# Performance work log

Measured on AMD Instinct MI355X. Metric: run time of the kernel, lower is better.

Reference implementation:

```python
import jax, jax.numpy as jnp
import numpy as np

B, S, H, D = 8, 1024, 8, 64      # batch, seq_len, num_heads, num_hidden
DM = H * D                        # input model dim = 512
DK = 64.0                         # d_k scale
EPS = 1e-3                        # keras GroupNormalization default epsilon


def setup_inputs() -> dict:
    key = jax.random.key(0)
    ks = jax.random.split(key, 12)
    sc = 1.0 / np.sqrt(DM)
    return {
        "query":  jax.random.normal(ks[0], (B, S, DM), jnp.float32),
        "key":    jax.random.normal(ks[1], (B, S, DM), jnp.float32),
        "values": jax.random.normal(ks[2], (B, S, DM), jnp.float32),
        "Wq": jax.random.normal(ks[3], (DM, 3 * H * D), jnp.float32) * sc,
        "bq": jnp.zeros((3 * H * D,), jnp.float32),
        "Wk": jax.random.normal(ks[4], (DM, 2 * H * D), jnp.float32) * sc,
        "bk": jnp.zeros((2 * H * D,), jnp.float32),
        "Wv": jax.random.normal(ks[5], (DM, H * D), jnp.float32) * sc,
        "bv": jnp.zeros((H * D,), jnp.float32),
        "gamma": jnp.ones((D,), jnp.float32),
        "beta": jnp.zeros((D,), jnp.float32),
        "lam": jax.random.uniform(ks[6], (1,), jnp.float32),          # trainable lambda
        "lambda_init": jax.random.uniform(ks[7], (1,), jnp.float32),  # frozen lambda_init
    }


def reference(query, key, values, Wq, bq, Wk, bk, Wv, bv, gamma, beta, lam, lambda_init):
    # projections -> (B, H, S, *)
    q = (query @ Wq + bq).reshape(B, S, H, 3 * D).transpose(0, 2, 1, 3)
    k = (key @ Wk + bk).reshape(B, S, H, 2 * D).transpose(0, 2, 1, 3)
    v = (values @ Wv + bv).reshape(B, S, H, D).transpose(0, 2, 1, 3)

    q1, q2, gate = jnp.split(q, 3, axis=-1)      # each (B,H,S,D)
    k1, k2 = k[..., :D], k[..., D:]

    inv = 1.0 / jnp.sqrt(jnp.float32(DK))
    s1 = jnp.einsum("bhqd,bhkd->bhqk", q1, k1) * inv
    s2 = jnp.einsum("bhqd,bhkd->bhqk", q2, k2) * inv

    # differential attention: dual softmax combined with learned lambda
    attn = jax.nn.softmax(s1, axis=-1) - lam[0] * jax.nn.softmax(s2, axis=-1)
    out = jnp.einsum("bhqk,bhkd->bhqd", attn, v)      # (B,H,S,D)
    out = out.transpose(0, 2, 1, 3)                    # (B,S,H,D)

    # keras GroupNormalization(groups=H, axis=-1) on channels D:
    # reshape channel dim into (groups, D//H), reduce over all non-batch,
    # non-group axes: (S, H, D//H)
    g = out.reshape(B, S, H, H, D // H)
    mean = jnp.mean(g, axis=(1, 2, 4), keepdims=True)
    var = jnp.var(g, axis=(1, 2, 4), keepdims=True)
    g = (g - mean) * jax.lax.rsqrt(var + EPS)
    out = g.reshape(B, S, H, D) * gamma + beta

    out = out * (1.0 - lambda_init[0])
    out = out * jax.nn.sigmoid(gate.transpose(0, 2, 1, 3))
    return out.reshape(B, S, H * D)
```

## Files before the change

### kernel.cpp

```cpp
#include <hip/hip_runtime.h>
#include <cstdint>
#include <cstddef>

#define B_ 8
#define S_ 1024
#define H_ 8
#define D_ 64
#define DM_ 512

typedef __bf16 bf16x8 __attribute__((ext_vector_type(8)));
typedef float floatx4 __attribute__((ext_vector_type(4)));
typedef float floatx16 __attribute__((ext_vector_type(16)));
typedef unsigned short ushort8 __attribute__((ext_vector_type(8)));
typedef unsigned short ushort4v __attribute__((ext_vector_type(4)));
typedef unsigned int uint32x2 __attribute__((ext_vector_type(2)));

union Frag { ushort8 us; bf16x8 bf; };

#define MFMA16(a, b, c) __builtin_amdgcn_mfma_f32_16x16x32_bf16((a), (b), (c), 0, 0, 0)
#define MFMA32(a, b, c) __builtin_amdgcn_mfma_f32_32x32x16_bf16((a), (b), (c), 0, 0, 0)

__device__ __forceinline__ unsigned short f2bf(float f) {
  unsigned int u = __float_as_uint(f);
  unsigned int r = (u + 0x7fffu + ((u >> 16) & 1u)) >> 16;
  return (unsigned short)r;
}

__device__ __forceinline__ uint32_t cvtpk_bf16(float lo, float hi) {
  uint32_t r;
  asm("v_cvt_pk_bf16_f32 %0, %1, %2" : "=v"(r) : "v"(lo), "v"(hi));
  return r;
}

__device__ __forceinline__ void gload16(const void* g, void* l) {
  __builtin_amdgcn_global_load_lds(
      (const __attribute__((address_space(1))) unsigned int*)g,
      (__attribute__((address_space(3))) unsigned int*)l, 16, 0, 0);
}

__global__ __launch_bounds__(256) void prep_kernel(
    const float* __restrict__ q, const float* __restrict__ k,
    const float* __restrict__ v, unsigned short* __restrict__ abf,
    const float* __restrict__ Wq, const float* __restrict__ Wk,
    const float* __restrict__ Wv, unsigned short* __restrict__ wt,
    float* __restrict__ partial)
{
  __shared__ unsigned short sT[64][72];
  const int tid = threadIdx.x;
  if (blockIdx.x < 2048) {
    const int t = blockIdx.x * 256 + tid;
    #pragma unroll
    for (int i = 0; i < 6; i++) {
      size_t i4 = ((size_t)i * 524288 + t) * 4;
      const size_t SEG = (size_t)4 << 20;
      const float* src = (i4 < SEG) ? (q + i4)
                       : (i4 < 2 * SEG) ? (k + (i4 - SEG))
                                        : (v + (i4 - 2 * SEG));
      floatx4 f = *(const floatx4*)src;
      ushort4v o;
      o[0] = f2bf(f[0]); o[1] = f2bf(f[1]); o[2] = f2bf(f[2]); o[3] = f2bf(f[3]);
      *(ushort4v*)(abf + i4) = o;
    }
    return;
  }
  if (blockIdx.x == 2432) {
    if (tid < 128) partial[tid] = 0.f;
    return;
  }
  const int bid = blockIdx.x - 2048;
  const int k0 = (bid & 7) * 64;
  const int n0 = (bid >> 3) * 64;
  const float* src; int ncols, nb;
  if (n0 < 1536)      { src = Wq; ncols = 1536; nb = n0; }
  else if (n0 < 2560) { src = Wk; ncols = 1024; nb = n0 - 1536; }
  else                { src = Wv; ncols = 512;  nb = n0 - 2560; }

  const int kr0 = tid >> 4, nc4 = (tid & 15) * 4;
  #pragma unroll
  for (int i = 0; i < 4; i++) {
    int kr = kr0 + i * 16;
    floatx4 f = *(const floatx4*)(src + (size_t)(k0 + kr) * ncols + nb + nc4);
    sT[nc4 + 0][kr] = f2bf(f[0]);
    sT[nc4 + 1][kr] = f2bf(f[1]);
    sT[nc4 + 2][kr] = f2bf(f[2]);
    sT[nc4 + 3][kr] = f2bf(f[3]);
  }
  __syncthreads();
  const int nr0 = tid >> 3, kc8 = (tid & 7) * 8;
  #pragma unroll
  for (int i = 0; i < 2; i++) {
    int nr = nr0 + i * 32;
    *(ushort8*)(wt + (size_t)(n0 + nr) * 512 + k0 + kc8) = *(const ushort8*)&sT[nr][kc8];
  }
}

__global__ __launch_bounds__(256) void gemm_kernel(
    const unsigned short* __restrict__ abf, const unsigned short* __restrict__ wt,
    const float* __restrict__ bq, const float* __restrict__ bk,
    const float* __restrict__ bv,
    unsigned short* __restrict__ q1, unsigned short* __restrict__ q2,
    float* __restrict__ gate, unsigned short* __restrict__ k1,
    unsigned short* __restrict__ k2, unsigned short* __restrict__ vT)
{
  const int tid  = threadIdx.x;
  const int wave = tid >> 6;
  const int lane = tid & 63;
  const int l16  = lane & 15;
  const int quad = lane >> 4;
  const int mt = blockIdx.x;
  const int nt = blockIdx.y;
  const int wm = wave & 1, wn = wave >> 1;

  const unsigned short* Asrc =
      abf + (nt < 12 ? 0 : nt < 20 ? ((size_t)4 << 20) : ((size_t)8 << 20));

  __shared__ unsigned short sMem[4 * 128 * 64];

  floatx4 acc[4][4];
  #pragma unroll
  for (int i = 0; i < 4; i++)
    #pragma unroll
    for (int j = 0; j < 4; j++)
      #pragma unroll
      for (int r = 0; r < 4; r++) acc[i][j][r] = 0.0f;

  const int lrow   = lane >> 3;
  const int gchunk = (lane & 7) ^ lrow;
  const int rkey   = l16 & 7;

  auto STAGE = [&](int kt, int buf) {
    unsigned short* sA = sMem + buf * 16384;
    unsigned short* sB = sA + 8192;
    #pragma unroll
    for (int j = 0; j < 4; j++) {
      int r8 = (wave * 4 + j) * 8;
      gload16(Asrc + (size_t)(mt * 128 + r8 + lrow) * 512 + kt * 64 + gchunk * 8,
              &sA[(wave * 4 + j) * 512]);
      gload16(wt + (size_t)(nt * 128 + r8 + lrow) * 512 + kt * 64 + gchunk * 8,
              &sB[(wave * 4 + j) * 512]);
    }
  };

  auto COMPUTE = [&](int buf) {
    unsigned short* sA = sMem + buf * 16384;
    unsigned short* sB = sA + 8192;
    #pragma unroll
    for (int c = 0; c < 2; c++) {
      Frag af[4], bf[4];
      #pragma unroll
      for (int mi = 0; mi < 4; mi++)
        af[mi].us = *(const ushort8*)&sA[(wm * 64 + mi * 16 + l16) * 64 +
                                         (((c * 4 + quad) ^ rkey) << 3)];
      #pragma unroll
      for (int ni = 0; ni < 4; ni++)
        bf[ni].us = *(const ushort8*)&sB[(wn * 64 + ni * 16 + l16) * 64 +
                                         (((c * 4 + quad) ^ rkey) << 3)];
      __builtin_amdgcn_s_setprio(1);
      #pragma unroll
      for (int mi = 0; mi < 4; mi++)
        #pragma unroll
        for (int ni = 0; ni < 4; ni++)
          acc[mi][ni] = MFMA16(af[mi].bf, bf[ni].bf, acc[mi][ni]);
      __builtin_amdgcn_s_setprio(0);
    }
  };

  STAGE(0, 0);
  asm volatile("s_waitcnt vmcnt(0)" ::: "memory");
  __builtin_amdgcn_s_barrier();
  for (int kt = 0; kt < 8; kt++) {
    if (kt < 7) STAGE(kt + 1, (kt + 1) & 1);
    COMPUTE(kt & 1);
    asm volatile("s_waitcnt vmcnt(0) lgkmcnt(0)" ::: "memory");
    __builtin_amdgcn_s_barrier();
  }

  const int gm0 = mt * 128 + wm * 64;
  const int bb  = gm0 >> 10;
  const int s0  = gm0 & 1023;
  const int nseg = nt * 2 + wn;
  unsigned short* sC = sMem + wave * 4096;

  int h, sel = 0; bool isV = false;
  const float* bias_arr; int nb0;
  unsigned short* dstb = nullptr;
  if (nseg < 24)      { h = nseg / 3; sel = nseg % 3; bias_arr = bq; nb0 = nseg * 64;
                        dstb = (sel == 0) ? q1 : (sel == 1) ? q2 : nullptr; }
  else if (nseg < 40) { int t = nseg - 24; h = t >> 1; sel = t & 1;
                        bias_arr = bk; nb0 = t * 64; dstb = sel ? k2 : k1; }
  else                { h = nseg - 40; isV = true; bias_arr = bv; nb0 = (nseg - 40) * 64; }

  if (dstb != nullptr || isV) {
    const float scl = (nseg < 24) ? 0.125f * 1.44269504088896f : 1.0f;
    #pragma unroll
    for (int ni = 0; ni < 4; ni++) {
      float bv_ = bias_arr[nb0 + ni * 16 + l16];
      #pragma unroll
      for (int mi = 0; mi < 4; mi++)
        #pragma unroll
        for (int r = 0; r < 4; r++) {
          float val = (acc[mi][ni][r] + bv_) * scl;
          int ml = mi * 16 + quad * 4 + r;
          int nl = ni * 16 + l16;
          if (!isV) {
            int ch = (nl >> 3) ^ (ml & 7);
            sC[ml * 64 + (ch << 3) + (nl & 7)] = f2bf(val);
          } else {
            int ch = (ml >> 3) ^ (nl & 7);
            sC[nl * 64 + (ch << 3) + (ml & 7)] = f2bf(val);
          }
        }
    }
    const int rr = lane >> 3, cc = lane & 7;
    if (!isV) {
      unsigned short* base = dstb + ((size_t)(bb * H_ + h) * S_ + s0) * D_;
      #pragma unroll
      for (int j = 0; j < 8; j++) {
        int row = j * 8 + rr;
        int logc = cc ^ (row & 7);
        ushort8 valv = *(const ushort8*)&sC[row * 64 + cc * 8];
        *(ushort8*)(base + (size_t)row * D_ + logc * 8) = valv;
      }
    } else {
      unsigned short* base = vT + ((size_t)(bb * H_ + h) * D_) * S_ + s0;
      #pragma unroll
      for (int j = 0; j < 8; j++) {
        int drow = j * 8 + rr;
        int logc = cc ^ (drow & 7);
        ushort8 valv = *(const ushort8*)&sC[drow * 64 + cc * 8];
        *(ushort8*)(base + (size_t)drow * S_ + logc * 8) = valv;
      }
    }
  } else {
    #pragma unroll
    for (int ni = 0; ni < 4; ni++) {
      float bv_ = bias_arr[nb0 + ni * 16 + l16];
      #pragma unroll
      for (int mi = 0; mi < 4; mi++)
        #pragma unroll
        for (int r = 0; r < 4; r++) {
          int s = s0 + mi * 16 + quad * 4 + r;
          int d = ni * 16 + l16;
          gate[((size_t)(bb * H_ + h) * S_ + s) * D_ + d] = acc[mi][ni][r] + bv_;
        }
    }
  }
}

__global__ __launch_bounds__(256, 4) void attn_kernel(
    const unsigned short* __restrict__ q1, const unsigned short* __restrict__ q2,
    const unsigned short* __restrict__ k1, const unsigned short* __restrict__ k2,
    const unsigned short* __restrict__ vT, const float* __restrict__ lamp,
    float* __restrict__ O, float* __restrict__ partial)
{
  const int tid   = threadIdx.x;
  const int wave  = tid >> 6;
  const int lane  = tid & 63;
  const int l32   = lane & 31;
  const int lhalf = lane >> 5;
  const int kh    = wave & 1;
  const int qh    = wave >> 1;
  const int bh = blockIdx.x & 63;
  const int qt = blockIdx.x >> 6;
  const int q0 = qt * 64;

  __shared__ unsigned short sMem[5 * 4096];
  unsigned short* sK1 = sMem;
  unsigned short* sK2 = sMem + 4096;
  unsigned short* sVt = sMem + 8192;
  unsigned short* sP1 = sMem + 12288;
  unsigned short* sP2 = sMem + 16384;

  const size_t qrowoff = ((size_t)bh * S_ + q0 + qh * 32 + l32) * D_ + lhalf * 8;
  Frag qb1[4], qb2[4];
  #pragma unroll
  for (int ks = 0; ks < 4; ks++) {
    qb1[ks].us = *(const ushort8*)(q1 + qrowoff + ks * 16);
    qb2[ks].us = *(const ushort8*)(q2 + qrowoff + ks * 16);
  }

  floatx16 o1, o2;
  #pragma unroll
  for (int r = 0; r < 16; r++) { o1[r] = 0.f; o2[r] = 0.f; }
  float l1 = 0.f, l2 = 0.f;

  const unsigned short* kb1 = k1 + (size_t)bh * S_ * D_;
  const unsigned short* kb2 = k2 + (size_t)bh * S_ * D_;
  const unsigned short* vb  = vT + (size_t)bh * D_ * S_;

  const int srow = lane >> 3;
  const int sgch = (lane & 7) ^ srow;
  const int akey = l32 & 7;
  const int mrow = kh * 32 + l32;
  const int qrow = (qh * 32 + l32) * 64;

  auto STAGE_K = [&](int kt) {
    #pragma unroll
    for (int i = 0; i < 2; i++) {
      int r0 = wave * 16 + i * 8;
      gload16(kb1 + (size_t)(kt * 64 + r0 + srow) * 64 + sgch * 8, &sK1[r0 * 64]);
      gload16(kb2 + (size_t)(kt * 64 + r0 + srow) * 64 + sgch * 8, &sK2[r0 * 64]);
    }
  };
  auto STAGE_V = [&](int kt) {
    #pragma unroll
    for (int i = 0; i < 2; i++) {
      int r0 = wave * 16 + i * 8;
      gload16(vb + (size_t)(r0 + srow) * S_ + kt * 64 + sgch * 8, &sVt[r0 * 64]);
    }
  };

  auto S_PHASE = [&]() {
    floatx16 s1, s2;
    #pragma unroll
    for (int r = 0; r < 16; r++) { s1[r] = 0.f; s2[r] = 0.f; }
    __builtin_amdgcn_s_setprio(1);
    #pragma unroll
    for (int ks = 0; ks < 4; ks++) {
      int phys = ((ks * 2 + lhalf) ^ akey) << 3;
      Frag kf1; kf1.us = *(const ushort8*)&sK1[mrow * 64 + phys];
      s1 = MFMA32(kf1.bf, qb1[ks].bf, s1);
      Frag kf2; kf2.us = *(const ushort8*)&sK2[mrow * 64 + phys];
      s2 = MFMA32(kf2.bf, qb2[ks].bf, s2);
    }
    __builtin_amdgcn_s_setprio(0);
    #pragma unroll
    for (int qd = 0; qd < 4; qd++) {
      const int addr = qrow + (((kh * 4 + qd) ^ akey) << 3) + 4 * lhalf;
      float e0 = __builtin_amdgcn_exp2f(s1[4 * qd + 0]);
      float e1 = __builtin_amdgcn_exp2f(s1[4 * qd + 1]);
      float e2 = __builtin_amdgcn_exp2f(s1[4 * qd + 2]);
      float e3 = __builtin_amdgcn_exp2f(s1[4 * qd + 3]);
      l1 += (e0 + e1) + (e2 + e3);
      uint32x2 w1; w1[0] = cvtpk_bf16(e0, e1); w1[1] = cvtpk_bf16(e2, e3);
      *(uint32x2*)&sP1[addr] = w1;
      float f0 = __builtin_amdgcn_exp2f(s2[4 * qd + 0]);
      float f1 = __builtin_amdgcn_exp2f(s2[4 * qd + 1]);
      float f2 = __builtin_amdgcn_exp2f(s2[4 * qd + 2]);
      float f3 = __builtin_amdgcn_exp2f(s2[4 * qd + 3]);
      l2 += (f0 + f1) + (f2 + f3);
      uint32x2 w2; w2[0] = cvtpk_bf16(f0, f1); w2[1] = cvtpk_bf16(f2, f3);
      *(uint32x2*)&sP2[addr] = w2;
    }
  };

  auto PV_PHASE = [&]() {
    __builtin_amdgcn_s_setprio(1);
    #pragma unroll
    for (int ks = 0; ks < 4; ks++) {
      int phys = ((ks * 2 + lhalf) ^ akey) << 3;
      Frag vf; vf.us = *(const ushort8*)&sVt[mrow * 64 + phys];
      Frag pf1; pf1.us = *(const ushort8*)&sP1[qrow + phys];
      o1 = MFMA32(vf.bf, pf1.bf, o1);
      Frag pf2; pf2.us = *(const ushort8*)&sP2[qrow + phys];
      o2 = MFMA32(vf.bf, pf2.bf, o2);
    }
    __builtin_amdgcn_s_setprio(0);
  };

  STAGE_K(0);
  STAGE_V(0);
  asm volatile("s_waitcnt vmcnt(2)" ::: "memory");
  __builtin_amdgcn_s_barrier();
  S_PHASE();
  asm volatile("s_waitcnt vmcnt(0) lgkmcnt(0)" ::: "memory");
  __builtin_amdgcn_s_barrier();

  for (int kt = 1; kt < 16; kt++) {
    STAGE_K(kt);
    PV_PHASE();
    asm volatile("s_waitcnt lgkmcnt(0)" ::: "memory");
    __builtin_amdgcn_s_barrier();
    STAGE_V(kt);
    asm volatile("s_waitcnt vmcnt(2)" ::: "memory");
    __builtin_amdgcn_s_barrier();
    S_PHASE();
    asm volatile("s_waitcnt vmcnt(0) lgkmcnt(0)" ::: "memory");
    __builtin_amdgcn_s_barrier();
  }
  PV_PHASE();
  asm volatile("s_waitcnt lgkmcnt(0)" ::: "memory");
  __builtin_amdgcn_s_barrier();

  l1 += __shfl_xor(l1, 32, 64);
  l2 += __shfl_xor(l2, 32, 64);
  float* sL = (float*)(sMem + 10240);
  float* sG = (float*)(sMem + 10752);
  if (lane < 32) {
    sL[(0 * 2 + kh) * 64 + qh * 32 + l32] = l1;
    sL[(1 * 2 + kh) * 64 + qh * 32 + l32] = l2;
  }
  __syncthreads();

  const int q = qh * 32 + l32;
  float i1 = 1.0f / (sL[q] + sL[64 + q]);
  float i2 = lamp[0] / (sL[128 + q] + sL[192 + q]);
  float* fO = (float*)sMem;
  #pragma unroll
  for (int r = 0; r < 16; r++) {
    int d = kh * 32 + (r & 3) + 8 * (r >> 2) + 4 * lhalf;
    fO[d * 65 + q] = o1[r] * i1 - o2[r] * i2;
  }
  if (tid < 16) sG[tid] = 0.f;
  __syncthreads();

  float ss = 0.f, ss2 = 0.f;
  float* Ob = O + ((size_t)bh * S_ + q0) * D_;
  #pragma unroll
  for (int i = 0; i < 4; i++) {
    int qrw = i * 16 + (tid >> 4);
    int d0 = (tid & 15) * 4;
    floatx4 v;
    #pragma unroll
    for (int j = 0; j < 4; j++) {
      v[j] = fO[(d0 + j) * 65 + qrw];
      ss += v[j]; ss2 += v[j] * v[j];
    }
    *(floatx4*)(Ob + (size_t)qrw * D_ + d0) = v;
  }
  ss  += __shfl_xor(ss, 16, 64);  ss  += __shfl_xor(ss, 32, 64);  ss  += __shfl_xor(ss, 1, 64);
  ss2 += __shfl_xor(ss2, 16, 64); ss2 += __shfl_xor(ss2, 32, 64); ss2 += __shfl_xor(ss2, 1, 64);
  if (lane < 16 && (lane & 1) == 0) {
    int j = lane >> 1;
    atomicAdd(&sG[j * 2],     ss);
    atomicAdd(&sG[j * 2 + 1], ss2);
  }
  __syncthreads();
  if (tid < 16) atomicAdd(&partial[(bh >> 3) * 16 + tid], sG[tid]);
}

__global__ __launch_bounds__(256) void final_kernel(
    const float* __restrict__ O, const float* __restrict__ gate,
    const float* __restrict__ partial, const float* __restrict__ gamma,
    const float* __restrict__ beta, const float* __restrict__ li,
    float* __restrict__ out)
{
  const int t = blockIdx.x * 256 + threadIdx.x;
  const float li0 = 1.0f - li[0];
  #pragma unroll
  for (int it = 0; it < 2; it++) {
    int e4 = (it * 524288 + t) * 4;
    int d0 = e4 & 63;
    int hh = (e4 >> 6) & 7;
    int s  = (e4 >> 9) & 1023;
    int b  = e4 >> 19;
    size_t oidx = (size_t)(b * 8 + hh) * 65536 + (size_t)s * 64 + d0;
    int g = b * 8 + (d0 >> 3);
    float S1 = partial[g * 2];
    float S2 = partial[g * 2 + 1];
    float mean = S1 * (1.0f / 65536.f);
    float inv  = rsqrtf(S2 * (1.0f / 65536.f) - mean * mean + 0.001f);
    floatx4 o  = *(const floatx4*)(O + oidx);
    floatx4 gt = *(const floatx4*)(gate + oidx);
    floatx4 gm = *(const floatx4*)(gamma + d0);
    floatx4 bt = *(const floatx4*)(beta + d0);
    floatx4 r;
    #pragma unroll
    for (int j = 0; j < 4; j++) {
      float x = (o[j] - mean) * inv;
      x = x * gm[j] + bt[j];
      x *= li0;
      x *= 1.0f / (1.0f + __expf(-gt[j]));
      r[j] = x;
    }
    *(floatx4*)(out + e4) = r;
  }
}

extern "C" void kernel_launch(void* const* d_in, const int* in_sizes, int n_in,
                              void* d_out, int out_size, void* d_ws, size_t ws_size,
                              hipStream_t stream)
{
  const float* query  = (const float*)d_in[0];
  const float* key    = (const float*)d_in[1];
  const float* values = (const float*)d_in[2];
  const float* Wq = (const float*)d_in[3];
  const float* bq = (const float*)d_in[4];
  const float* Wk = (const float*)d_in[5];
  const float* bk = (const float*)d_in[6];
  const float* Wv = (const float*)d_in[7];
  const float* bv = (const float*)d_in[8];
  const float* gamma = (const float*)d_in[9];
  const float* beta  = (const float*)d_in[10];
  const float* lam   = (const float*)d_in[11];
  const float* lami  = (const float*)d_in[12];
  float* out = (float*)d_out;

  char* ws = (char*)d_ws;
  const size_t MB = (size_t)1 << 20;
  unsigned short* abf = (unsigned short*)(ws);
  float*          O   = (float*)(ws);
  unsigned short* wt  = (unsigned short*)(ws + 24 * MB);
  float* partial      = (float*)(ws + 27 * MB);
  unsigned short* q1  = (unsigned short*)(ws + 28 * MB);
  unsigned short* q2  = (unsigned short*)(ws + 36 * MB);
  unsigned short* k1  = (unsigned short*)(ws + 44 * MB);
  unsigned short* k2  = (unsigned short*)(ws + 52 * MB);
  unsigned short* vT  = (unsigned short*)(ws + 60 * MB);
  float* gate         = (float*)(ws + 68 * MB);

  prep_kernel<<<2433, 256, 0, stream>>>(query, key, values, abf, Wq, Wk, Wv, wt,
                                        partial);
  gemm_kernel<<<dim3(64, 24), 256, 0, stream>>>(abf, wt, bq, bk, bv,
                                                q1, q2, gate, k1, k2, vT);
  attn_kernel<<<dim3(1024), 256, 0, stream>>>(q1, q2, k1, k2, vT, lam, O, partial);
  final_kernel<<<2048, 256, 0, stream>>>(O, gate, partial, gamma, beta, lami, out);
}
```

Measured before the change: 220.7 us.

## Fuse fp32-to-bf16 activation conversion into GEMM A-tile loading

Removes the separate prep pass that converted the fp32 query/key/value activations to bf16 in a workspace. The GEMM now loads fp32 A tiles into registers, converts them to bf16, and writes them to LDS in the already-swizzled layout, while B still streams through global_load_lds. This avoids writing and re-reading a 24MB bf16 intermediate. In exchange the GEMM reads twice the A bytes, each A row is re-read across 12/8/4 N tiles, and the convert-and-store step now sits on the pipeline's critical path with extra register pressure.

```diff
diff --git a/kernel.cpp b/kernel.cpp
--- a/kernel.cpp
+++ b/kernel.cpp
@@ -39,35 +39,17 @@
 }
 
 __global__ __launch_bounds__(256) void prep_kernel(
-    const float* __restrict__ q, const float* __restrict__ k,
-    const float* __restrict__ v, unsigned short* __restrict__ abf,
     const float* __restrict__ Wq, const float* __restrict__ Wk,
     const float* __restrict__ Wv, unsigned short* __restrict__ wt,
     float* __restrict__ partial)
 {
   __shared__ unsigned short sT[64][72];
   const int tid = threadIdx.x;
-  if (blockIdx.x < 2048) {
-    const int t = blockIdx.x * 256 + tid;
-    #pragma unroll
-    for (int i = 0; i < 6; i++) {
-      size_t i4 = ((size_t)i * 524288 + t) * 4;
-      const size_t SEG = (size_t)4 << 20;
-      const float* src = (i4 < SEG) ? (q + i4)
-                       : (i4 < 2 * SEG) ? (k + (i4 - SEG))
-                                        : (v + (i4 - 2 * SEG));
-      floatx4 f = *(const floatx4*)src;
-      ushort4v o;
-      o[0] = f2bf(f[0]); o[1] = f2bf(f[1]); o[2] = f2bf(f[2]); o[3] = f2bf(f[3]);
-      *(ushort4v*)(abf + i4) = o;
-    }
-    return;
-  }
-  if (blockIdx.x == 2432) {
+  if (blockIdx.x == 384) {
     if (tid < 128) partial[tid] = 0.f;
     return;
   }
-  const int bid = blockIdx.x - 2048;
+  const int bid = blockIdx.x;
   const int k0 = (bid & 7) * 64;
   const int n0 = (bid >> 3) * 64;
   const float* src; int ncols, nb;
@@ -95,7 +77,8 @@
 }
 
 __global__ __launch_bounds__(256) void gemm_kernel(
-    const unsigned short* __restrict__ abf, const unsigned short* __restrict__ wt,
+    const float* __restrict__ qf, const float* __restrict__ kf,
+    const float* __restrict__ vf, const unsigned short* __restrict__ wt,
     const float* __restrict__ bq, const float* __restrict__ bk,
     const float* __restrict__ bv,
     unsigned short* __restrict__ q1, unsigned short* __restrict__ q2,
@@ -111,8 +94,7 @@
   const int nt = blockIdx.y;
   const int wm = wave & 1, wn = wave >> 1;
 
-  const unsigned short* Asrc =
-      abf + (nt < 12 ? 0 : nt < 20 ? ((size_t)4 << 20) : ((size_t)8 << 20));
+  const float* Af = (nt < 12) ? qf : (nt < 20) ? kf : vf;
 
   __shared__ unsigned short sMem[4 * 128 * 64];
 
@@ -128,14 +110,34 @@
   const int gchunk = (lane & 7) ^ lrow;
   const int rkey   = l16 & 7;
 
-  auto STAGE = [&](int kt, int buf) {
-    unsigned short* sA = sMem + buf * 16384;
-    unsigned short* sB = sA + 8192;
+  floatx4 fA[4][2];
+
+  auto LOADA = [&](int kt) {
     #pragma unroll
     for (int j = 0; j < 4; j++) {
       int r8 = (wave * 4 + j) * 8;
-      gload16(Asrc + (size_t)(mt * 128 + r8 + lrow) * 512 + kt * 64 + gchunk * 8,
-              &sA[(wave * 4 + j) * 512]);
+      const float* ga = Af + (size_t)(mt * 128 + r8 + lrow) * 512 + kt * 64 + gchunk * 8;
+      fA[j][0] = *(const floatx4*)ga;
+      fA[j][1] = *(const floatx4*)(ga + 4);
+    }
+  };
+  auto WRITEA = [&](int buf) {
+    unsigned short* sA = sMem + buf * 16384;
+    #pragma unroll
+    for (int j = 0; j < 4; j++) {
+      ushort8 o;
+      o[0] = f2bf(fA[j][0][0]); o[1] = f2bf(fA[j][0][1]);
+      o[2] = f2bf(fA[j][0][2]); o[3] = f2bf(fA[j][0][3]);
+      o[4] = f2bf(fA[j][1][0]); o[5] = f2bf(fA[j][1][1]);
+      o[6] = f2bf(fA[j][1][2]); o[7] = f2bf(fA[j][1][3]);
+      *(ushort8*)&sA[(wave * 4 + j) * 512 + lane * 8] = o;
+    }
+  };
+  auto STAGE_B = [&](int kt, int buf) {
+    unsigned short* sB = sMem + buf * 16384 + 8192;
+    #pragma unroll
+    for (int j = 0; j < 4; j++) {
+      int r8 = (wave * 4 + j) * 8;
       gload16(wt + (size_t)(nt * 128 + r8 + lrow) * 512 + kt * 64 + gchunk * 8,
               &sB[(wave * 4 + j) * 512]);
     }
@@ -165,13 +167,21 @@
     }
   };
 
-  STAGE(0, 0);
+  LOADA(0);
+  STAGE_B(0, 0);
   asm volatile("s_waitcnt vmcnt(0)" ::: "memory");
+  WRITEA(0);
+  asm volatile("s_waitcnt lgkmcnt(0)" ::: "memory");
   __builtin_amdgcn_s_barrier();
+
   for (int kt = 0; kt < 8; kt++) {
-    if (kt < 7) STAGE(kt + 1, (kt + 1) & 1);
+    if (kt < 7) { LOADA(kt + 1); STAGE_B(kt + 1, (kt + 1) & 1); }
     COMPUTE(kt & 1);
-    asm volatile("s_waitcnt vmcnt(0) lgkmcnt(0)" ::: "memory");
+    if (kt < 7) {
+      asm volatile("s_waitcnt vmcnt(0)" ::: "memory");
+      WRITEA((kt + 1) & 1);
+    }
+    asm volatile("s_waitcnt lgkmcnt(0)" ::: "memory");
     __builtin_amdgcn_s_barrier();
   }
 
@@ -488,7 +498,6 @@
 
   char* ws = (char*)d_ws;
   const size_t MB = (size_t)1 << 20;
-  unsigned short* abf = (unsigned short*)(ws);
   float*          O   = (float*)(ws);
   unsigned short* wt  = (unsigned short*)(ws + 24 * MB);
   float* partial      = (float*)(ws + 27 * MB);
@@ -499,9 +508,9 @@
   unsigned short* vT  = (unsigned short*)(ws + 60 * MB);
   float* gate         = (float*)(ws + 68 * MB);
 
-  prep_kernel<<<2433, 256, 0, stream>>>(query, key, values, abf, Wq, Wk, Wv, wt,
-                                        partial);
-  gemm_kernel<<<dim3(64, 24), 256, 0, stream>>>(abf, wt, bq, bk, bv,
+  prep_kernel<<<385, 256, 0, stream>>>(Wq, Wk, Wv, wt, partial);
+  gemm_kernel<<<dim3(64, 24), 256, 0, stream>>>(query, key, values, wt,
+                                                bq, bk, bv,
                                                 q1, q2, gate, k1, k2, vT);
   attn_kernel<<<dim3(1024), 256, 0, stream>>>(q1, q2, k1, k2, vT, lam, O, partial);
   final_kernel<<<2048, 256, 0, stream>>>(O, gate, partial, gamma, beta, lami, out);
```

Result: no change. 223.3 us (+1.2%).
